# Optimization experiments

Measured on AMD Instinct MI355X. Metric: run time of the kernel, lower is better.

The kernel has to match this reference:

```python
import jax, jax.numpy as jnp
import numpy as np

ALPHA = 0.1
K_HOPS = 16


def mlp_readout(y, ws, bs):
    # MLPReadout with L=2: two relu layers then linear
    for w, b in zip(ws[:-1], bs[:-1]):
        y = jax.nn.relu(y @ w.T + b)
    return y @ ws[-1].T + bs[-1]


def gru_dir(xs, w_ih, w_hh, b_ih, b_hh, reverse):
    # xs: [B, T, D]; PyTorch GRU cell semantics
    H = w_hh.shape[1]
    def cell(h, xt):
        gi = xt @ w_ih.T + b_ih            # [B, 3H]
        gh = h @ w_hh.T + b_hh             # [B, 3H]
        i_r, i_z, i_n = jnp.split(gi, 3, -1)
        h_r, h_z, h_n = jnp.split(gh, 3, -1)
        r = jax.nn.sigmoid(i_r + h_r)
        z = jax.nn.sigmoid(i_z + h_z)
        n = jnp.tanh(i_n + r * h_n)
        h2 = (1.0 - z) * n + z * h
        return h2, h2
    h0 = jnp.zeros((xs.shape[0], H), xs.dtype)
    _, ys = jax.lax.scan(cell, h0, jnp.swapaxes(xs, 0, 1), reverse=reverse)
    return jnp.swapaxes(ys, 0, 1)          # [B, T, H]


def appnp(x, edge_index):
    # APPNP with GCN symmetric normalization and self-loops
    N = x.shape[0]
    loop = jnp.arange(N, dtype=edge_index.dtype)
    src = jnp.concatenate([edge_index[0], loop])
    dst = jnp.concatenate([edge_index[1], loop])
    deg = jax.ops.segment_sum(jnp.ones(src.shape, x.dtype), dst, num_segments=N)
    dinv = jax.lax.rsqrt(jnp.maximum(deg, 1.0))
    w = (dinv[src] * dinv[dst])[:, None]    # [E+N, 1]
    def step(z, _):
        m = jax.ops.segment_sum(z[src] * w, dst, num_segments=N)
        return (1.0 - ALPHA) * m + ALPHA * x, None
    z, _ = jax.lax.scan(step, x, None, length=K_HOPS)
    return z


def setup_inputs():
    key = jax.random.key(0)
    ks = jax.random.split(key, 24)
    N, D, E, B, T, S, Hs, C = 20000, 768, 200000, 64, 128, 128, 512, 14
    sc = 0.05
    p = {}
    p['x'] = jax.random.normal(ks[0], (N, D), jnp.float32)
    p['edge_index'] = jax.random.randint(ks[1], (2, E), 0, N, dtype=jnp.int32).astype(jnp.int64)
    p['sequence'] = jax.random.normal(ks[2], (B, T, S), jnp.float32)
    p['batch'] = jnp.sort(jax.random.randint(ks[3], (N,), 0, B, dtype=jnp.int32)).astype(jnp.int64)
    # BiGRU params (forward / backward directions)
    p['gru_wih_f'] = jax.random.normal(ks[4], (3 * Hs, S), jnp.float32) * sc
    p['gru_whh_f'] = jax.random.normal(ks[5], (3 * Hs, Hs), jnp.float32) * sc
    p['gru_bih_f'] = jax.random.normal(ks[6], (3 * Hs,), jnp.float32) * sc
    p['gru_bhh_f'] = jax.random.normal(ks[7], (3 * Hs,), jnp.float32) * sc
    p['gru_wih_b'] = jax.random.normal(ks[8], (3 * Hs, S), jnp.float32) * sc
    p['gru_whh_b'] = jax.random.normal(ks[9], (3 * Hs, Hs), jnp.float32) * sc
    p['gru_bih_b'] = jax.random.normal(ks[10], (3 * Hs,), jnp.float32) * sc
    p['gru_bhh_b'] = jax.random.normal(ks[11], (3 * Hs,), jnp.float32) * sc
    # mlp_graph: 768 -> 384 -> 192 -> 14
    p['mg_w0'] = jax.random.normal(ks[12], (384, 768), jnp.float32) * sc
    p['mg_b0'] = jnp.zeros((384,), jnp.float32)
    p['mg_w1'] = jax.random.normal(ks[13], (192, 384), jnp.float32) * sc
    p['mg_b1'] = jnp.zeros((192,), jnp.float32)
    p['mg_w2'] = jax.random.normal(ks[14], (C, 192), jnp.float32) * sc
    p['mg_b2'] = jnp.zeros((C,), jnp.float32)
    # mlp_seq: 1024 -> 512 -> 256 -> 14
    p['ms_w0'] = jax.random.normal(ks[15], (512, 1024), jnp.float32) * sc
    p['ms_b0'] = jnp.zeros((512,), jnp.float32)
    p['ms_w1'] = jax.random.normal(ks[16], (256, 512), jnp.float32) * sc
    p['ms_b1'] = jnp.zeros((256,), jnp.float32)
    p['ms_w2'] = jax.random.normal(ks[17], (C, 256), jnp.float32) * sc
    p['ms_b2'] = jnp.zeros((C,), jnp.float32)
    return p


def reference(x, edge_index, sequence, batch,
              gru_wih_f, gru_whh_f, gru_bih_f, gru_bhh_f,
              gru_wih_b, gru_whh_b, gru_bih_b, gru_bhh_b,
              mg_w0, mg_b0, mg_w1, mg_b1, mg_w2, mg_b2,
              ms_w0, ms_b0, ms_w1, ms_b1, ms_w2, ms_b2):
    B = sequence.shape[0]
    # BiGRU over sequence (dropout is identity in eval mode)
    fwd = gru_dir(sequence, gru_wih_f, gru_whh_f, gru_bih_f, gru_bhh_f, False)
    bwd = gru_dir(sequence, gru_wih_b, gru_whh_b, gru_bih_b, gru_bhh_b, True)
    seq_out = jnp.concatenate([fwd, bwd], axis=-1)   # [B, T, 2H]
    seq1 = jnp.mean(seq_out, axis=1)                 # avg_pool over time
    seq2 = jnp.max(seq_out, axis=1)                  # max_pool over time
    seq_logits = mlp_readout(seq1 + seq2, [ms_w0, ms_w1, ms_w2], [ms_b0, ms_b1, ms_b2])
    # APPNP K-hop sparse propagation + global mean pool
    z = appnp(x, edge_index)
    cnt = jnp.maximum(jax.ops.segment_sum(jnp.ones((x.shape[0],), x.dtype), batch, num_segments=B), 1.0)
    pooled = jax.ops.segment_sum(z, batch, num_segments=B) / cnt[:, None]
    g_logits = mlp_readout(pooled, [mg_w0, mg_w1, mg_w2], [mg_b0, mg_b1, mg_b2])
    return g_logits + seq_logits
```

## Files before the change

kernel.cpp:

```cpp
#include <hip/hip_runtime.h>
#include <stdint.h>

#define ALPHA 0.1f
#define NN 20000
#define DF 768
#define NE 200000
#define NB 64
#define TSEQ 128
#define SF 128
#define HS 512
#define NCLS 14

typedef __attribute__((ext_vector_type(8))) short short8;
typedef __attribute__((ext_vector_type(4))) float f32x4;
typedef __attribute__((ext_vector_type(4))) unsigned int u32x4;

#define OFF_DEG     0u
#define OFF_CSRC    80000u
#define OFF_CNTB    160000u
#define OFF_FLAG64  176640u
#define ZERO_INTS   44161u
#define OFF_ROWPTR  176896u
#define OFF_CURSOR  257024u
#define OFF_DINV    337024u
#define OFF_COL     417024u
#define OFF_WGT     1217024u
#define OFF_V0      2017280u
#define OFF_V1      7137280u
#define OFF_HBUF    12257280u
#define OFF_HFLAG   12519424u
#define OFF_YSEQ    12781568u
#define OFF_SH1     13043712u
#define OFF_SH2     13174784u
#define OFF_PART    13240320u
#define OFF_POOL    16386048u
#define OFF_GH1     16582656u
#define OFF_GH2     16680960u

__device__ __forceinline__ unsigned short f2b(float f) {
  union { float f; unsigned u; } v; v.f = f;
  unsigned u = v.u;
  return (unsigned short)((u + 0x7FFFu + ((u >> 16) & 1u)) >> 16);
}

__device__ __forceinline__ int idx_at(const int* p, long long i, int mode64) {
  return mode64 ? p[2*i] : p[i];
}

__global__ void zero_ints_kernel(int* p, int n) {
  int i = blockIdx.x * blockDim.x + threadIdx.x;
  if (i < n) p[i] = 0;
}

__global__ void detect_i64_kernel(const int* e, int* flag) {
  int lane = threadIdx.x;
  int ok = 1;
  for (int i = lane; i < 256; i += 64) ok &= (e[2 * i + 1] == 0);
  ok = __all(ok);
  if (lane == 0 && blockIdx.x == 0) *flag = ok ? 1 : 0;
}

__global__ void hist_kernel(const int* e, const int* batch, int* deg, int* csrc,
                            int* cntb, const int* flag) {
  int i = blockIdx.x * blockDim.x + threadIdx.x;
  int m = *flag;
  if (i < NE) {
    int s = idx_at(e, i, m);
    int d = idx_at(e, (long long)NE + i, m);
    atomicAdd(&csrc[s], 1);
    atomicAdd(&deg[d], 1);
  }
  if (i < NN) atomicAdd(&cntb[idx_at(batch, i, m)], 1);
}

__global__ void dinv_kernel(const int* deg, float* dinv) {
  int i = blockIdx.x * blockDim.x + threadIdx.x;
  if (i < NN) dinv[i] = rsqrtf((float)(deg[i] + 1));
}

__global__ void scan_kernel(const int* cnt, int* row_ptr, int* cursor) {
  __shared__ int sA[1024], sB[1024];
  int tid = threadIdx.x;
  int carry = 0;
  const int nch = (NN + 1023) / 1024;
  for (int c = 0; c < nch; ++c) {
    int i = c * 1024 + tid;
    int v = (i < NN) ? cnt[i] : 0;
    sA[tid] = v;
    __syncthreads();
    int* src = sA; int* dst = sB;
    for (int off = 1; off < 1024; off <<= 1) {
      dst[tid] = src[tid] + (tid >= off ? src[tid - off] : 0);
      __syncthreads();
      int* t = src; src = dst; dst = t;
    }
    if (i < NN) { int ex = carry + src[tid] - v; row_ptr[i] = ex; cursor[i] = ex; }
    carry += src[1023];
    __syncthreads();
  }
  if (tid == 0) row_ptr[NN] = carry;
}

__global__ void fill_kernel(const int* e, const float* dinv, int* cursor,
                            int* colA, float* wgt, const int* flag) {
  int i = blockIdx.x * blockDim.x + threadIdx.x;
  if (i >= NE) return;
  int m = *flag;
  int s = idx_at(e, i, m);
  int d = idx_at(e, (long long)NE + i, m);
  int pos = atomicAdd(&cursor[s], 1);
  colA[pos] = d;
  wgt[pos] = dinv[s] * dinv[d];
}

__global__ void v0init_kernel(const int* batch, float* v0, const int* flag) {
  int i = blockIdx.x * blockDim.x + threadIdx.x;
  if (i >= NN * 64) return;
  int n = i >> 6, b = i & 63;
  v0[i] = (idx_at(batch, n, *flag) == b) ? 1.0f : 0.0f;
}

__global__ __launch_bounds__(256) void hop_kernel(
    const float* __restrict__ vin, float* __restrict__ vout,
    const int* __restrict__ row_ptr, const int* __restrict__ colA,
    const float* __restrict__ wgt, const float* __restrict__ dinv,
    const int* __restrict__ batch, const int* __restrict__ flag) {
  int wid = (blockIdx.x * blockDim.x + threadIdx.x) >> 6;
  int lane = threadIdx.x & 63;
  if (wid >= NN) return;
  const int quad = lane >> 4, l15 = lane & 15;
  const int c4 = l15 * 4;
  float di = dinv[wid];
  int e0 = __builtin_amdgcn_readfirstlane(row_ptr[wid]);
  int e1 = __builtin_amdgcn_readfirstlane(row_ptr[wid + 1]);

  float ax, ay, az, aw;
  {
    float w = (quad == 0) ? di * di : 0.0f;
    const float* vr = vin + (size_t)wid * 64 + c4;
    ax = w * vr[0]; ay = w * vr[1]; az = w * vr[2]; aw = w * vr[3];
  }
  for (int e = e0; e < e1; e += 8) {
    int i0 = e + quad, i1 = e + 4 + quad;
    int a0 = (i0 < e1), a1 = (i1 < e1);
    int j0 = a0 ? i0 : e0;
    int j1 = a1 ? i1 : e0;
    int cc0 = colA[j0];
    int cc1 = colA[j1];
    float w0 = a0 ? wgt[j0] : 0.0f;
    float w1 = a1 ? wgt[j1] : 0.0f;
    const float* p0 = vin + (size_t)cc0 * 64 + c4;
    const float* p1 = vin + (size_t)cc1 * 64 + c4;
    float v00 = p0[0], v01 = p0[1], v02 = p0[2], v03 = p0[3];
    float v10 = p1[0], v11 = p1[1], v12 = p1[2], v13 = p1[3];
    ax += w0 * v00 + w1 * v10;
    ay += w0 * v01 + w1 * v11;
    az += w0 * v02 + w1 * v12;
    aw += w0 * v03 + w1 * v13;
  }
  ax += __shfl_xor(ax, 16); ax += __shfl_xor(ax, 32);
  ay += __shfl_xor(ay, 16); ay += __shfl_xor(ay, 32);
  az += __shfl_xor(az, 16); az += __shfl_xor(az, 32);
  aw += __shfl_xor(aw, 16); aw += __shfl_xor(aw, 32);
  if (quad == 0) {
    int b = idx_at(batch, wid, *flag);
    float* o = vout + (size_t)wid * 64 + c4;
    float4 r;
    r.x = (1.0f - ALPHA) * ax + ((b == c4 + 0) ? ALPHA : 0.0f);
    r.y = (1.0f - ALPHA) * ay + ((b == c4 + 1) ? ALPHA : 0.0f);
    r.z = (1.0f - ALPHA) * az + ((b == c4 + 2) ? ALPHA : 0.0f);
    r.w = (1.0f - ALPHA) * aw + ((b == c4 + 3) ? ALPHA : 0.0f);
    *(float4*)o = r;
  }
}

__global__ void spmm_kernel(const float* __restrict__ S, const float* __restrict__ x,
                            float* __restrict__ partial) {
  int wid = (blockIdx.x * blockDim.x + threadIdx.x) >> 6;
  int lane = threadIdx.x & 63;
  int ft = wid % 48, ch = wid / 48;
  if (ch >= 16) return;
  int f0 = ft * 16;
  int n0 = ch * 1250, n1 = n0 + 1250;
  float acc[16];
#pragma unroll
  for (int f = 0; f < 16; ++f) acc[f] = 0.0f;
  for (int n = n0; n < n1; ++n) {
    float sv = S[n * 64 + lane];
    const float* xr = x + (size_t)n * DF + f0;
#pragma unroll
    for (int f = 0; f < 16; ++f) acc[f] += sv * xr[f];
  }
  float* pr = partial + ((size_t)(ch * 64 + lane)) * DF + f0;
#pragma unroll
  for (int f = 0; f < 16; ++f) pr[f] = acc[f];
}

__global__ void reduce_pool_kernel(const float* __restrict__ partial, const int* __restrict__ cntb,
                                   float* __restrict__ pooled) {
  int i = blockIdx.x * blockDim.x + threadIdx.x;
  if (i >= 64 * DF) return;
  int b = i / DF, f = i - b * DF;
  float s = 0.0f;
  for (int c = 0; c < 16; ++c) s += partial[((size_t)(c * 64 + b)) * DF + f];
  int cnt = cntb[b]; if (cnt < 1) cnt = 1;
  pooled[i] = s / (float)cnt;
}

__global__ void mlp_layer_kernel(const float* __restrict__ A, const float* __restrict__ W,
                                 const float* __restrict__ bias, float* __restrict__ C,
                                 int M, int N, int K, int relu, int accum) {
  int i = blockIdx.x * blockDim.x + threadIdx.x;
  if (i >= M * N) return;
  int mrow = i / N, n = i - mrow * N;
  float acc = bias[n];
  const float4* a4 = (const float4*)(A + (size_t)mrow * K);
  const float4* w4 = (const float4*)(W + (size_t)n * K);
  int k4 = K >> 2;
#pragma unroll 4
  for (int k = 0; k < k4; ++k) {
    float4 av = a4[k], wv = w4[k];
    acc += av.x * wv.x + av.y * wv.y + av.z * wv.z + av.w * wv.w;
  }
  if (relu) acc = fmaxf(acc, 0.0f);
  if (accum) C[i] += acc; else C[i] = acc;
}

__global__ __launch_bounds__(64, 1) void gru_kernel(
    const float* __restrict__ seq,
    const float* __restrict__ wih_f, const float* __restrict__ whh_f,
    const float* __restrict__ bih_f, const float* __restrict__ bhh_f,
    const float* __restrict__ wih_b, const float* __restrict__ whh_b,
    const float* __restrict__ bih_b, const float* __restrict__ bhh_b,
    unsigned* __restrict__ hbuf, unsigned* __restrict__ hflag,
    float* __restrict__ y_seq) {
  __shared__ unsigned short hl[8 * 648];

  const int lane = threadIdx.x;
  const int quad = lane >> 4, l15 = lane & 15;
  const int d  = blockIdx.x >> 8;
  const int g  = (blockIdx.x >> 5) & 7;
  const int rk = blockIdx.x & 31;
  const int seqbase = g * 8;
  const int c0 = rk * 16;

  const float* WHHd = d ? whh_b : whh_f;
  const float* WIHd = d ? wih_b : wih_f;
  const float* BIHd = d ? bih_b : bih_f;
  const float* BHHd = d ? bhh_b : bhh_f;

  auto ldw = [&](int gcol, int j) -> short8 {
    int k0 = j * 32 + quad * 8;
    const float* p = (k0 < 512) ? (WHHd + (size_t)gcol * 512 + k0)
                                : (WIHd + (size_t)gcol * 128 + (k0 - 512));
    float4 f0 = *(const float4*)p;
    float4 f1 = *(const float4*)(p + 4);
    short8 r;
    r[0] = (short)f2b(f0.x); r[1] = (short)f2b(f0.y);
    r[2] = (short)f2b(f0.z); r[3] = (short)f2b(f0.w);
    r[4] = (short)f2b(f1.x); r[5] = (short)f2b(f1.y);
    r[6] = (short)f2b(f1.z); r[7] = (short)f2b(f1.w);
    return r;
  };
  short8 wr[20], wz[20], wn[20];
#pragma unroll
  for (int j = 0; j < 20; ++j) {
    wr[j] = ldw(c0 + l15, j);
    wz[j] = ldw(512 + c0 + l15, j);
    wn[j] = ldw(1024 + c0 + l15, j);
  }

  auto stage_x = [&](int t_x) {
    int tt = d ? (127 - t_x) : t_x;
    int s = lane >> 3, k0 = (lane & 7) * 16;
    const float* sp = seq + (size_t)(seqbase + s) * (TSEQ * SF) + tt * SF + k0;
    float4 a = *(const float4*)sp;
    float4 b = *(const float4*)(sp + 4);
    float4 c = *(const float4*)(sp + 8);
    float4 e = *(const float4*)(sp + 12);
    unsigned* xq = (unsigned*)(hl + s * 648 + 512 + k0);
    xq[0] = (unsigned)f2b(a.x) | ((unsigned)f2b(a.y) << 16);
    xq[1] = (unsigned)f2b(a.z) | ((unsigned)f2b(a.w) << 16);
    xq[2] = (unsigned)f2b(b.x) | ((unsigned)f2b(b.y) << 16);
    xq[3] = (unsigned)f2b(b.z) | ((unsigned)f2b(b.w) << 16);
    xq[4] = (unsigned)f2b(c.x) | ((unsigned)f2b(c.y) << 16);
    xq[5] = (unsigned)f2b(c.z) | ((unsigned)f2b(c.w) << 16);
    xq[6] = (unsigned)f2b(e.x) | ((unsigned)f2b(e.y) << 16);
    xq[7] = (unsigned)f2b(e.z) | ((unsigned)f2b(e.w) << 16);
  };

  for (int i = lane; i < 8 * 512; i += 64)
    hl[(i >> 9) * 648 + (i & 511)] = 0;
  stage_x(0);

  const float b_r  = BIHd[c0 + l15] + BHHd[c0 + l15];
  const float b_z  = BIHd[512 + c0 + l15] + BHHd[512 + c0 + l15];
  const float b_in = BIHd[1024 + c0 + l15];
  const float b_hn = BHHd[1024 + c0 + l15];

  float hprev[4] = {0, 0, 0, 0};
  float msum[4]  = {0, 0, 0, 0};
  float mxv[4]   = {-1e30f, -1e30f, -1e30f, -1e30f};

  for (int t = 0; t < 128; ++t) {
    f32x4 ar = {0, 0, 0, 0}, az = {0, 0, 0, 0};
    f32x4 anh = {0, 0, 0, 0}, anx = {0, 0, 0, 0};
    const unsigned short* arow = hl + (l15 & 7) * 648 + quad * 8;
#pragma unroll
    for (int kc = 0; kc < 20; ++kc) {
      short8 af = *(const short8*)(arow + kc * 32);
      ar = __builtin_amdgcn_mfma_f32_16x16x32_bf16(af, wr[kc], ar, 0, 0, 0);
      az = __builtin_amdgcn_mfma_f32_16x16x32_bf16(af, wz[kc], az, 0, 0, 0);
      if (kc < 16)
        anh = __builtin_amdgcn_mfma_f32_16x16x32_bf16(af, wn[kc], anh, 0, 0, 0);
      else
        anx = __builtin_amdgcn_mfma_f32_16x16x32_bf16(af, wn[kc], anx, 0, 0, 0);
    }

    float h2v[4];
#pragma unroll
    for (int rr = 0; rr < 4; ++rr) {
      float r = 1.0f / (1.0f + __expf(-(ar[rr] + b_r)));
      float z = 1.0f / (1.0f + __expf(-(az[rr] + b_z)));
      float narg = anx[rr] + b_in + r * (anh[rr] + b_hn);
      float e2 = __expf(-2.0f * fabsf(narg));
      float nt = (1.0f - e2) / (1.0f + e2);
      nt = (narg < 0.0f) ? -nt : nt;
      float h2 = (1.0f - z) * nt + z * hprev[rr];
      hprev[rr] = h2; msum[rr] += h2; mxv[rr] = fmaxf(mxv[rr], h2);
      h2v[rr] = h2;
    }

    if (t < 127) {
      const int slot = (t + 1) & 1;
      const unsigned tag = (unsigned)(t + 1);
#pragma unroll
      for (int rr = 0; rr < 4; ++rr) {
        unsigned me = f2b(h2v[rr]);
        unsigned nb = (unsigned)__shfl_xor((int)me, 1);
        if (lane < 32 && !(lane & 1)) {
          int row = (lane >> 4) * 4 + rr;
          unsigned word = (me & 0xFFFFu) | (nb << 16);
          unsigned* dp = hbuf +
              ((size_t)((slot * 2 + d) * 64 + seqbase + row)) * 256 +
              (unsigned)((c0 + (lane & 15)) >> 1);
          asm volatile("global_store_dword %0, %1, off sc0 sc1"
                       :: "v"(dp), "v"(word) : "memory");
        }
      }
      asm volatile("s_waitcnt vmcnt(0)" ::: "memory");
      if (lane == 0) {
        unsigned* fpo = hflag + ((size_t)(slot * 2 + d) * 8 + g) * 64 + rk;
        unsigned tv = tag;
        asm volatile("global_store_dword %0, %1, off sc0 sc1"
                     :: "v"(fpo), "v"(tv) : "memory");
      }
      stage_x(t + 1);
      const unsigned* fp = hflag + ((size_t)(slot * 2 + d) * 8 + g) * 64 + (lane & 31);
      int guard = 0;
      unsigned fv;
      for (;;) {
        asm volatile("global_load_dword %0, %1, off sc0 sc1"
                     : "=v"(fv) : "v"(fp) : "memory");
        asm volatile("s_waitcnt vmcnt(0)" ::: "memory");
        __builtin_amdgcn_sched_barrier(0);
        if (__all(fv == tag)) break;
        if (++guard > (1 << 20)) break;
        __builtin_amdgcn_s_sleep(1);
      }
      const unsigned* db = hbuf + (size_t)((slot * 2 + d) * 64 + seqbase) * 256;
      u32x4 w[8];
#pragma unroll
      for (int c = 0; c < 8; ++c)
        asm volatile("global_load_dwordx4 %0, %1, off sc0 sc1"
                     : "=v"(w[c]) : "v"(db + c * 256 + lane * 4) : "memory");
      asm volatile("s_waitcnt vmcnt(0)" ::: "memory");
      __builtin_amdgcn_sched_barrier(0);
#pragma unroll
      for (int c = 0; c < 8; ++c) {
        unsigned* dp = (unsigned*)(hl + c * 648) + lane * 4;
        dp[0] = w[c][0]; dp[1] = w[c][1]; dp[2] = w[c][2]; dp[3] = w[c][3];
      }
    }
  }

  if (lane < 32) {
#pragma unroll
    for (int rr = 0; rr < 4; ++rr) {
      int row = (lane >> 4) * 4 + rr;
      y_seq[(size_t)(seqbase + row) * 1024 + d * 512 + c0 + l15] =
          msum[rr] * (1.0f / 128.0f) + mxv[rr];
    }
  }
}

extern "C" void kernel_launch(void* const* d_in, const int* in_sizes, int n_in,
                              void* d_out, int out_size, void* d_ws, size_t ws_size,
                              hipStream_t stream) {
  const float* x      = (const float*)d_in[0];
  const int*   eidx   = (const int*)d_in[1];
  const float* seq    = (const float*)d_in[2];
  const int*   batch  = (const int*)d_in[3];
  const float* wih_f  = (const float*)d_in[4];
  const float* whh_f  = (const float*)d_in[5];
  const float* bih_f  = (const float*)d_in[6];
  const float* bhh_f  = (const float*)d_in[7];
  const float* wih_b  = (const float*)d_in[8];
  const float* whh_b  = (const float*)d_in[9];
  const float* bih_b  = (const float*)d_in[10];
  const float* bhh_b  = (const float*)d_in[11];
  const float* mg_w0  = (const float*)d_in[12];
  const float* mg_b0  = (const float*)d_in[13];
  const float* mg_w1  = (const float*)d_in[14];
  const float* mg_b1  = (const float*)d_in[15];
  const float* mg_w2  = (const float*)d_in[16];
  const float* mg_b2  = (const float*)d_in[17];
  const float* ms_w0  = (const float*)d_in[18];
  const float* ms_b0  = (const float*)d_in[19];
  const float* ms_w1  = (const float*)d_in[20];
  const float* ms_b1  = (const float*)d_in[21];
  const float* ms_w2  = (const float*)d_in[22];
  const float* ms_b2  = (const float*)d_in[23];
  float* out = (float*)d_out;
  char* ws = (char*)d_ws;

  int*   deg     = (int*)(ws + OFF_DEG);
  int*   csrc    = (int*)(ws + OFF_CSRC);
  int*   cntb    = (int*)(ws + OFF_CNTB);
  int*   flag    = (int*)(ws + OFF_FLAG64);
  int*   row_ptr = (int*)(ws + OFF_ROWPTR);
  int*   cursor  = (int*)(ws + OFF_CURSOR);
  float* dinv    = (float*)(ws + OFF_DINV);
  int*   colA    = (int*)(ws + OFF_COL);
  float* wgtA    = (float*)(ws + OFF_WGT);
  float* V0      = (float*)(ws + OFF_V0);
  float* V1      = (float*)(ws + OFF_V1);
  unsigned* hbuf = (unsigned*)(ws + OFF_HBUF);
  unsigned* hflag= (unsigned*)(ws + OFF_HFLAG);
  float* y_seq   = (float*)(ws + OFF_YSEQ);
  float* sh1     = (float*)(ws + OFF_SH1);
  float* sh2     = (float*)(ws + OFF_SH2);
  float* part    = (float*)(ws + OFF_PART);
  float* pooled  = (float*)(ws + OFF_POOL);
  float* gh1     = (float*)(ws + OFF_GH1);
  float* gh2     = (float*)(ws + OFF_GH2);

  zero_ints_kernel<<<(ZERO_INTS + 255) / 256, 256, 0, stream>>>((int*)ws, (int)ZERO_INTS);
  zero_ints_kernel<<<8, 256, 0, stream>>>((int*)(ws + OFF_HFLAG), 2048);
  detect_i64_kernel<<<1, 64, 0, stream>>>(eidx, flag);
  hist_kernel<<<(NE + 255) / 256, 256, 0, stream>>>(eidx, batch, deg, csrc, cntb, flag);
  dinv_kernel<<<(NN + 255) / 256, 256, 0, stream>>>(deg, dinv);
  scan_kernel<<<1, 1024, 0, stream>>>(csrc, row_ptr, cursor);
  fill_kernel<<<(NE + 255) / 256, 256, 0, stream>>>(eidx, dinv, cursor, colA, wgtA, flag);
  v0init_kernel<<<(NN * 64 + 255) / 256, 256, 0, stream>>>(batch, V0, flag);

  for (int h = 0; h < 16; ++h) {
    const float* vin = (h & 1) ? V1 : V0;
    float* vout = (h & 1) ? V0 : V1;
    hop_kernel<<<(NN * 64 + 255) / 256, 256, 0, stream>>>(vin, vout, row_ptr, colA,
                                                          wgtA, dinv, batch, flag);
  }

  gru_kernel<<<512, 64, 0, stream>>>(
      seq, wih_f, whh_f, bih_f, bhh_f, wih_b, whh_b, bih_b, bhh_b, hbuf, hflag, y_seq);

  mlp_layer_kernel<<<(64 * 512 + 255) / 256, 256, 0, stream>>>(y_seq, ms_w0, ms_b0, sh1,
                                                               64, 512, 1024, 1, 0);
  mlp_layer_kernel<<<(64 * 256 + 255) / 256, 256, 0, stream>>>(sh1, ms_w1, ms_b1, sh2,
                                                               64, 256, 512, 1, 0);
  mlp_layer_kernel<<<(64 * NCLS + 255) / 256, 256, 0, stream>>>(sh2, ms_w2, ms_b2, out,
                                                                64, NCLS, 256, 0, 0);

  spmm_kernel<<<(768 * 64) / 256, 256, 0, stream>>>(V0, x, part);
  reduce_pool_kernel<<<(64 * DF + 255) / 256, 256, 0, stream>>>(part, cntb, pooled);

  mlp_layer_kernel<<<(64 * 384 + 255) / 256, 256, 0, stream>>>(pooled, mg_w0, mg_b0, gh1,
                                                               64, 384, 768, 1, 0);
  mlp_layer_kernel<<<(64 * 192 + 255) / 256, 256, 0, stream>>>(gh1, mg_w1, mg_b1, gh2,
                                                               64, 192, 384, 1, 0);
  mlp_layer_kernel<<<(64 * NCLS + 255) / 256, 256, 0, stream>>>(gh2, mg_w2, mg_b2, out,
                                                                64, NCLS, 192, 0, 1);
  (void)in_sizes; (void)n_in; (void)out_size; (void)ws_size;
}
```

Before: 1.529 ms.

## Fuse setup kernels, parallelize scan, and fuse MLP readouts per batch row

Merges the two zeroing launches, folds dinv, V0 init and a multi-block prefix scan into one combo kernel using per-chunk counts from the histogram, and restructures spmm with an intra-block reduction. It also replaces the six MLP layer launches plus the pool reduction with two per-row fused MLP kernels that keep hidden activations in shared memory. The goal is fewer launches, less serial scan work and less global traffic for intermediates. The cost is that the graph output now adds into out with atomicAdd, which depends on mlp_seq_kernel having written out first, and the MLP runs on only 64 blocks.

```diff
diff --git a/kernel.cpp b/kernel.cpp
--- a/kernel.cpp
+++ b/kernel.cpp
@@ -18,6 +18,7 @@
 #define OFF_DEG     0u
 #define OFF_CSRC    80000u
 #define OFF_CNTB    160000u
+#define OFF_CHT     160512u
 #define OFF_FLAG64  176640u
 #define ZERO_INTS   44161u
 #define OFF_ROWPTR  176896u
@@ -30,12 +31,9 @@
 #define OFF_HBUF    12257280u
 #define OFF_HFLAG   12519424u
 #define OFF_YSEQ    12781568u
-#define OFF_SH1     13043712u
-#define OFF_SH2     13174784u
 #define OFF_PART    13240320u
 #define OFF_POOL    16386048u
 #define OFF_GH1     16582656u
-#define OFF_GH2     16680960u
 
 __device__ __forceinline__ unsigned short f2b(float f) {
   union { float f; unsigned u; } v; v.f = f;
@@ -47,9 +45,15 @@
   return mode64 ? p[2*i] : p[i];
 }
 
-__global__ void zero_ints_kernel(int* p, int n) {
+__device__ __forceinline__ float dot4(float4 a, float4 b) {
+  return a.x * b.x + a.y * b.y + a.z * b.z + a.w * b.w;
+}
+
+__global__ void zero2_kernel(int* p1, int n1, int* p2, int n2) {
   int i = blockIdx.x * blockDim.x + threadIdx.x;
-  if (i < n) p[i] = 0;
+  if (i < n1) p1[i] = 0;
+  int j = i - n1;
+  if (j >= 0 && j < n2) p2[j] = 0;
 }
 
 __global__ void detect_i64_kernel(const int* e, int* flag) {
@@ -61,31 +65,33 @@
 }
 
 __global__ void hist_kernel(const int* e, const int* batch, int* deg, int* csrc,
-                            int* cntb, const int* flag) {
+                            int* cht, int* cntb, const int* flag) {
   int i = blockIdx.x * blockDim.x + threadIdx.x;
   int m = *flag;
   if (i < NE) {
     int s = idx_at(e, i, m);
     int d = idx_at(e, (long long)NE + i, m);
     atomicAdd(&csrc[s], 1);
+    atomicAdd(&cht[s / 1000], 1);
     atomicAdd(&deg[d], 1);
   }
   if (i < NN) atomicAdd(&cntb[idx_at(batch, i, m)], 1);
 }
 
-__global__ void dinv_kernel(const int* deg, float* dinv) {
-  int i = blockIdx.x * blockDim.x + threadIdx.x;
-  if (i < NN) dinv[i] = rsqrtf((float)(deg[i] + 1));
-}
-
-__global__ void scan_kernel(const int* cnt, int* row_ptr, int* cursor) {
-  __shared__ int sA[1024], sB[1024];
-  int tid = threadIdx.x;
-  int carry = 0;
-  const int nch = (NN + 1023) / 1024;
-  for (int c = 0; c < nch; ++c) {
-    int i = c * 1024 + tid;
-    int v = (i < NN) ? cnt[i] : 0;
+__global__ __launch_bounds__(1024) void combo_kernel(
+    const int* __restrict__ csrc, const int* __restrict__ cht,
+    const int* __restrict__ deg, int* __restrict__ row_ptr,
+    int* __restrict__ cursor, float* __restrict__ dinv,
+    const int* __restrict__ batch, const int* __restrict__ flag,
+    float* __restrict__ v0) {
+  const int tid = threadIdx.x, b = blockIdx.x;
+  if (b < 20) {
+    __shared__ int sA[1024], sB[1024];
+    int carry = 0;
+    for (int j = 0; j < b; ++j) carry += cht[j];
+    int i = b * 1000 + tid;
+    int active = (tid < 1000);
+    int v = active ? csrc[i] : 0;
     sA[tid] = v;
     __syncthreads();
     int* src = sA; int* dst = sB;
@@ -94,11 +100,20 @@
       __syncthreads();
       int* t = src; src = dst; dst = t;
     }
-    if (i < NN) { int ex = carry + src[tid] - v; row_ptr[i] = ex; cursor[i] = ex; }
-    carry += src[1023];
-    __syncthreads();
-  }
-  if (tid == 0) row_ptr[NN] = carry;
+    if (active) {
+      int ex = carry + src[tid] - v;
+      row_ptr[i] = ex; cursor[i] = ex;
+      dinv[i] = rsqrtf((float)(deg[i] + 1));
+    }
+    if (b == 19 && tid == 0) row_ptr[NN] = carry + src[999];
+  } else {
+    int m = *flag;
+    long long j = (long long)(b - 20) * 1024 + tid;
+    if (j < (long long)NN * 64) {
+      int n = (int)(j >> 6), gb = (int)(j & 63);
+      v0[j] = (idx_at(batch, n, m) == gb) ? 1.0f : 0.0f;
+    }
+  }
 }
 
 __global__ void fill_kernel(const int* e, const float* dinv, int* cursor,
@@ -111,13 +126,6 @@
   int pos = atomicAdd(&cursor[s], 1);
   colA[pos] = d;
   wgt[pos] = dinv[s] * dinv[d];
-}
-
-__global__ void v0init_kernel(const int* batch, float* v0, const int* flag) {
-  int i = blockIdx.x * blockDim.x + threadIdx.x;
-  if (i >= NN * 64) return;
-  int n = i >> 6, b = i & 63;
-  v0[i] = (idx_at(batch, n, *flag) == b) ? 1.0f : 0.0f;
 }
 
 __global__ __launch_bounds__(256) void hop_kernel(
@@ -174,56 +182,139 @@
   }
 }
 
-__global__ void spmm_kernel(const float* __restrict__ S, const float* __restrict__ x,
-                            float* __restrict__ partial) {
-  int wid = (blockIdx.x * blockDim.x + threadIdx.x) >> 6;
-  int lane = threadIdx.x & 63;
-  int ft = wid % 48, ch = wid / 48;
-  if (ch >= 16) return;
+__global__ __launch_bounds__(256) void spmm_kernel(
+    const float* __restrict__ S, const float* __restrict__ x,
+    float* __restrict__ partial) {
+  __shared__ float red[4][64][17];
+  int tid = threadIdx.x;
+  int w = tid >> 6, lane = tid & 63;
+  int beta = blockIdx.x;
+  int ft = beta % 48, cg = beta / 48;
+  int ch = cg * 4 + w;
   int f0 = ft * 16;
-  int n0 = ch * 1250, n1 = n0 + 1250;
+  int n0 = (ch * NN) >> 6, n1 = ((ch + 1) * NN) >> 6;
   float acc[16];
 #pragma unroll
   for (int f = 0; f < 16; ++f) acc[f] = 0.0f;
   for (int n = n0; n < n1; ++n) {
     float sv = S[n * 64 + lane];
-    const float* xr = x + (size_t)n * DF + f0;
-#pragma unroll
-    for (int f = 0; f < 16; ++f) acc[f] += sv * xr[f];
-  }
-  float* pr = partial + ((size_t)(ch * 64 + lane)) * DF + f0;
-#pragma unroll
-  for (int f = 0; f < 16; ++f) pr[f] = acc[f];
-}
-
-__global__ void reduce_pool_kernel(const float* __restrict__ partial, const int* __restrict__ cntb,
-                                   float* __restrict__ pooled) {
-  int i = blockIdx.x * blockDim.x + threadIdx.x;
-  if (i >= 64 * DF) return;
-  int b = i / DF, f = i - b * DF;
-  float s = 0.0f;
-  for (int c = 0; c < 16; ++c) s += partial[((size_t)(c * 64 + b)) * DF + f];
+    const float4* xr = (const float4*)(x + (size_t)n * DF + f0);
+    float4 x0 = xr[0], x1 = xr[1], x2 = xr[2], x3 = xr[3];
+    acc[0] += sv * x0.x; acc[1] += sv * x0.y; acc[2] += sv * x0.z; acc[3] += sv * x0.w;
+    acc[4] += sv * x1.x; acc[5] += sv * x1.y; acc[6] += sv * x1.z; acc[7] += sv * x1.w;
+    acc[8] += sv * x2.x; acc[9] += sv * x2.y; acc[10] += sv * x2.z; acc[11] += sv * x2.w;
+    acc[12] += sv * x3.x; acc[13] += sv * x3.y; acc[14] += sv * x3.z; acc[15] += sv * x3.w;
+  }
+#pragma unroll
+  for (int f = 0; f < 16; ++f) red[w][lane][f] = acc[f];
+  __syncthreads();
+#pragma unroll
+  for (int ff = 0; ff < 4; ++ff) {
+    int f = w * 4 + ff;
+    float s = red[0][lane][f] + red[1][lane][f] + red[2][lane][f] + red[3][lane][f];
+    partial[((size_t)(cg * 64 + lane)) * DF + f0 + f] = s;
+  }
+}
+
+__global__ __launch_bounds__(256) void mlp_seq_kernel(
+    const float* __restrict__ y_seq,
+    const float* __restrict__ w0, const float* __restrict__ b0,
+    const float* __restrict__ w1, const float* __restrict__ b1,
+    const float* __restrict__ w2, const float* __restrict__ b2,
+    float* __restrict__ out) {
+  __shared__ float a0[1024], h1[512], h2[256];
+  const int tid = threadIdx.x, b = blockIdx.x;
+  ((float4*)a0)[tid] = ((const float4*)(y_seq + (size_t)b * 1024))[tid];
+  __syncthreads();
+  {
+    int n = tid * 2;
+    float acc0 = b0[n], acc1 = b0[n + 1];
+    const float4* wa = (const float4*)(w0 + (size_t)n * 1024);
+    const float4* wb = wa + 256;
+#pragma unroll 4
+    for (int k = 0; k < 256; ++k) {
+      float4 av = ((float4*)a0)[k];
+      acc0 += dot4(av, wa[k]);
+      acc1 += dot4(av, wb[k]);
+    }
+    h1[n] = fmaxf(acc0, 0.0f);
+    h1[n + 1] = fmaxf(acc1, 0.0f);
+  }
+  __syncthreads();
+  {
+    float acc = b1[tid];
+    const float4* wa = (const float4*)(w1 + (size_t)tid * 512);
+#pragma unroll 4
+    for (int k = 0; k < 128; ++k) acc += dot4(((float4*)h1)[k], wa[k]);
+    h2[tid] = fmaxf(acc, 0.0f);
+  }
+  __syncthreads();
+  if (tid < 224) {
+    int o = tid >> 4, l = tid & 15;
+    const float4* wa = (const float4*)(w2 + (size_t)o * 256);
+    float part = 0.0f;
+#pragma unroll
+    for (int k = l; k < 64; k += 16) part += dot4(((float4*)h2)[k], wa[k]);
+    part += __shfl_xor(part, 1); part += __shfl_xor(part, 2);
+    part += __shfl_xor(part, 4); part += __shfl_xor(part, 8);
+    if (l == 0) out[b * NCLS + o] = part + b2[o];
+  }
+}
+
+__global__ __launch_bounds__(256) void mlp_graph_kernel(
+    const float* __restrict__ partial, const int* __restrict__ cntb,
+    const float* __restrict__ w0, const float* __restrict__ b0,
+    const float* __restrict__ w1, const float* __restrict__ b1,
+    const float* __restrict__ w2, const float* __restrict__ b2,
+    float* __restrict__ out) {
+  __shared__ float a0[768], h1[384], h2[192];
+  const int tid = threadIdx.x, b = blockIdx.x;
   int cnt = cntb[b]; if (cnt < 1) cnt = 1;
-  pooled[i] = s / (float)cnt;
-}
-
-__global__ void mlp_layer_kernel(const float* __restrict__ A, const float* __restrict__ W,
-                                 const float* __restrict__ bias, float* __restrict__ C,
-                                 int M, int N, int K, int relu, int accum) {
-  int i = blockIdx.x * blockDim.x + threadIdx.x;
-  if (i >= M * N) return;
-  int mrow = i / N, n = i - mrow * N;
-  float acc = bias[n];
-  const float4* a4 = (const float4*)(A + (size_t)mrow * K);
-  const float4* w4 = (const float4*)(W + (size_t)n * K);
-  int k4 = K >> 2;
+  const float cinv = 1.0f / (float)cnt;
+  if (tid < 192) {
+    float4 s = {0, 0, 0, 0};
+#pragma unroll
+    for (int c = 0; c < 16; ++c) {
+      float4 p = ((const float4*)(partial + ((size_t)(c * 64 + b)) * DF))[tid];
+      s.x += p.x; s.y += p.y; s.z += p.z; s.w += p.w;
+    }
+    s.x *= cinv; s.y *= cinv; s.z *= cinv; s.w *= cinv;
+    ((float4*)a0)[tid] = s;
+  }
+  __syncthreads();
+  if (tid < 192) {
+    int n = tid * 2;
+    float acc0 = b0[n], acc1 = b0[n + 1];
+    const float4* wa = (const float4*)(w0 + (size_t)n * 768);
+    const float4* wb = wa + 192;
 #pragma unroll 4
-  for (int k = 0; k < k4; ++k) {
-    float4 av = a4[k], wv = w4[k];
-    acc += av.x * wv.x + av.y * wv.y + av.z * wv.z + av.w * wv.w;
-  }
-  if (relu) acc = fmaxf(acc, 0.0f);
-  if (accum) C[i] += acc; else C[i] = acc;
+    for (int k = 0; k < 192; ++k) {
+      float4 av = ((float4*)a0)[k];
+      acc0 += dot4(av, wa[k]);
+      acc1 += dot4(av, wb[k]);
+    }
+    h1[n] = fmaxf(acc0, 0.0f);
+    h1[n + 1] = fmaxf(acc1, 0.0f);
+  }
+  __syncthreads();
+  if (tid < 192) {
+    float acc = b1[tid];
+    const float4* wa = (const float4*)(w1 + (size_t)tid * 384);
+#pragma unroll 4
+    for (int k = 0; k < 96; ++k) acc += dot4(((float4*)h1)[k], wa[k]);
+    h2[tid] = fmaxf(acc, 0.0f);
+  }
+  __syncthreads();
+  if (tid < 224) {
+    int o = tid >> 4, l = tid & 15;
+    const float4* wa = (const float4*)(w2 + (size_t)o * 192);
+    float part = 0.0f;
+#pragma unroll
+    for (int k = l; k < 48; k += 16) part += dot4(((float4*)h2)[k], wa[k]);
+    part += __shfl_xor(part, 1); part += __shfl_xor(part, 2);
+    part += __shfl_xor(part, 4); part += __shfl_xor(part, 8);
+    if (l == 0) atomicAdd(&out[b * NCLS + o], part + b2[o]);
+  }
 }
 
 __global__ __launch_bounds__(64, 1) void gru_kernel(
@@ -427,6 +518,7 @@
   int*   deg     = (int*)(ws + OFF_DEG);
   int*   csrc    = (int*)(ws + OFF_CSRC);
   int*   cntb    = (int*)(ws + OFF_CNTB);
+  int*   cht     = (int*)(ws + OFF_CHT);
   int*   flag    = (int*)(ws + OFF_FLAG64);
   int*   row_ptr = (int*)(ws + OFF_ROWPTR);
   int*   cursor  = (int*)(ws + OFF_CURSOR);
@@ -438,21 +530,16 @@
   unsigned* hbuf = (unsigned*)(ws + OFF_HBUF);
   unsigned* hflag= (unsigned*)(ws + OFF_HFLAG);
   float* y_seq   = (float*)(ws + OFF_YSEQ);
-  float* sh1     = (float*)(ws + OFF_SH1);
-  float* sh2     = (float*)(ws + OFF_SH2);
   float* part    = (float*)(ws + OFF_PART);
-  float* pooled  = (float*)(ws + OFF_POOL);
-  float* gh1     = (float*)(ws + OFF_GH1);
-  float* gh2     = (float*)(ws + OFF_GH2);
-
-  zero_ints_kernel<<<(ZERO_INTS + 255) / 256, 256, 0, stream>>>((int*)ws, (int)ZERO_INTS);
-  zero_ints_kernel<<<8, 256, 0, stream>>>((int*)(ws + OFF_HFLAG), 2048);
+
+  zero2_kernel<<<(ZERO_INTS + 2048 + 255) / 256, 256, 0, stream>>>(
+      (int*)ws, (int)ZERO_INTS, (int*)(ws + OFF_HFLAG), 2048);
   detect_i64_kernel<<<1, 64, 0, stream>>>(eidx, flag);
-  hist_kernel<<<(NE + 255) / 256, 256, 0, stream>>>(eidx, batch, deg, csrc, cntb, flag);
-  dinv_kernel<<<(NN + 255) / 256, 256, 0, stream>>>(deg, dinv);
-  scan_kernel<<<1, 1024, 0, stream>>>(csrc, row_ptr, cursor);
+  hist_kernel<<<(NE + 255) / 256, 256, 0, stream>>>(eidx, batch, deg, csrc, cht,
+                                                    cntb, flag);
+  combo_kernel<<<20 + (NN * 64 + 1023) / 1024, 1024, 0, stream>>>(
+      csrc, cht, deg, row_ptr, cursor, dinv, batch, flag, V0);
   fill_kernel<<<(NE + 255) / 256, 256, 0, stream>>>(eidx, dinv, cursor, colA, wgtA, flag);
-  v0init_kernel<<<(NN * 64 + 255) / 256, 256, 0, stream>>>(batch, V0, flag);
 
   for (int h = 0; h < 16; ++h) {
     const float* vin = (h & 1) ? V1 : V0;
@@ -461,24 +548,14 @@
                                                           wgtA, dinv, batch, flag);
   }
 
+  spmm_kernel<<<768, 256, 0, stream>>>(V0, x, part);
+
   gru_kernel<<<512, 64, 0, stream>>>(
       seq, wih_f, whh_f, bih_f, bhh_f, wih_b, whh_b, bih_b, bhh_b, hbuf, hflag, y_seq);
 
-  mlp_layer_kernel<<<(64 * 512 + 255) / 256, 256, 0, stream>>>(y_seq, ms_w0, ms_b0, sh1,
-                                                               64, 512, 1024, 1, 0);
-  mlp_layer_kernel<<<(64 * 256 + 255) / 256, 256, 0, stream>>>(sh1, ms_w1, ms_b1, sh2,
-                                                               64, 256, 512, 1, 0);
-  mlp_layer_kernel<<<(64 * NCLS + 255) / 256, 256, 0, stream>>>(sh2, ms_w2, ms_b2, out,
-                                                                64, NCLS, 256, 0, 0);
-
-  spmm_kernel<<<(768 * 64) / 256, 256, 0, stream>>>(V0, x, part);
-  reduce_pool_kernel<<<(64 * DF + 255) / 256, 256, 0, stream>>>(part, cntb, pooled);
-
-  mlp_layer_kernel<<<(64 * 384 + 255) / 256, 256, 0, stream>>>(pooled, mg_w0, mg_b0, gh1,
-                                                               64, 384, 768, 1, 0);
-  mlp_layer_kernel<<<(64 * 192 + 255) / 256, 256, 0, stream>>>(gh1, mg_w1, mg_b1, gh2,
-                                                               64, 192, 384, 1, 0);
-  mlp_layer_kernel<<<(64 * NCLS + 255) / 256, 256, 0, stream>>>(gh2, mg_w2, mg_b2, out,
-                                                                64, NCLS, 192, 0, 1);
+  mlp_seq_kernel<<<64, 256, 0, stream>>>(y_seq, ms_w0, ms_b0, ms_w1, ms_b1,
+                                         ms_w2, ms_b2, out);
+  mlp_graph_kernel<<<64, 256, 0, stream>>>(part, cntb, mg_w0, mg_b0, mg_w1, mg_b1,
+                                           mg_w2, mg_b2, out);
   (void)in_sizes; (void)n_in; (void)out_size; (void)ws_size;
 }
```

After: 1.627 ms. 6.4% more time.
